# Kernel optimization log

Measured on AMD Instinct MI355X. Metric: run time of the kernel, lower is better.

The kernel has to match this reference:

```python
import jax, jax.numpy as jnp
import numpy as np
from jax import lax

KS = 3
N = KS ** 3  # 27 kernel taps


def setup_inputs() -> dict:
    key = jax.random.key(0)
    k1, k2, k3 = jax.random.split(key, 3)
    B, Cin, Cout, D, H, W = 1, 32, 32, 32, 48, 48
    x = jax.random.normal(k1, (B, Cin, D, H, W), jnp.float32)
    # offset conv: 81 = 3*27 output channels, no bias (nn.Conv3d(..., bias=False))
    w_off = jax.random.normal(k2, (3 * N, Cin, KS, KS, KS), jnp.float32) * 0.01
    # deform conv kernel (bias defaults to None -> no bias)
    w_def = jax.random.normal(k3, (Cout, Cin, KS, KS, KS), jnp.float32) / np.sqrt(Cin * N)
    return {"x": x, "w_off": w_off, "w_def": w_def}


def _deform_block(x, w_off, w_def):
    B, C, D, H, W = x.shape
    dt = x.dtype

    # standard dense offset conv, padding=1
    offsets = lax.conv_general_dilated(
        x, w_off, (1, 1, 1), [(1, 1), (1, 1), (1, 1)],
        dimension_numbers=("NCDHW", "OIDHW", "NCDHW"))
    off = jnp.transpose(offsets, (0, 2, 3, 4, 1))  # (B,D,H,W,3N)
    od, oh, ow = off[..., :N], off[..., N:2 * N], off[..., 2 * N:]

    # zero-pad input (ConstantPad3d(1))
    xp = jnp.pad(x, ((0, 0), (0, 0), (1, 1), (1, 1), (1, 1)))
    Dp, Hp, Wp = D + 2, H + 2, W + 2

    # p_n: kernel grid offsets in (kd,kh,kw) row-major order, matching conv-weight layout
    r = jnp.arange(-(KS // 2), KS // 2 + 1, dtype=dt)
    pn = jnp.stack(jnp.meshgrid(r, r, r, indexing="ij"), 0).reshape(3, N)
    # p_0: centers in padded coordinates (1..D etc.)
    p0d = jnp.arange(1, D + 1, dtype=dt)[:, None, None, None]
    p0h = jnp.arange(1, H + 1, dtype=dt)[None, :, None, None]
    p0w = jnp.arange(1, W + 1, dtype=dt)[None, None, :, None]

    pd = p0d + pn[0] + od  # (B,D,H,W,N) sampling coords
    ph = p0h + pn[1] + oh
    pw = p0w + pn[2] + ow

    # integer corners (detached in original)
    fd = lax.stop_gradient(jnp.floor(pd))
    fh = lax.stop_gradient(jnp.floor(ph))
    fw = lax.stop_gradient(jnp.floor(pw))
    qd0 = jnp.clip(fd, 0, Dp - 1); qd1 = jnp.clip(fd + 1, 0, Dp - 1)
    qh0 = jnp.clip(fh, 0, Hp - 1); qh1 = jnp.clip(fh + 1, 0, Hp - 1)
    qw0 = jnp.clip(fw, 0, Wp - 1); qw1 = jnp.clip(fw + 1, 0, Wp - 1)

    # clip p to valid range (as in reference impl)
    pd = jnp.clip(pd, 0, Dp - 1)
    ph = jnp.clip(ph, 0, Hp - 1)
    pw = jnp.clip(pw, 0, Wp - 1)

    # trilinear weights per axis: g = 1 - |q - p|
    gd0 = 1 + (qd0 - pd); gd1 = 1 - (qd1 - pd)
    gh0 = 1 + (qh0 - ph); gh1 = 1 - (qh1 - ph)
    gw0 = 1 + (qw0 - pw); gw1 = 1 - (qw1 - pw)

    xf = xp.reshape(B, C, Dp * Hp * Wp)

    def gather(idd, ihh, iww):
        lin = ((idd.astype(jnp.int32) * Hp + ihh.astype(jnp.int32)) * Wp
               + iww.astype(jnp.int32)).reshape(B, 1, -1)
        v = jnp.take_along_axis(xf, jnp.broadcast_to(lin, (B, C, lin.shape[-1])), axis=2)
        return v.reshape(B, C, D, H, W, N)

    x_off = jnp.zeros((B, C, D, H, W, N), dt)
    for gd, idd in ((gd0, qd0), (gd1, qd1)):
        for gh, ihh in ((gh0, qh0), (gh1, qh1)):
            for gw, iww in ((gw0, qw0), (gw1, qw1)):
                x_off = x_off + (gd * gh * gw)[:, None] * gather(idd, ihh, iww)

    # stride-ks conv over reshaped x_offset == weighted sum over the N taps
    Cout = w_def.shape[0]
    out = jnp.einsum("bcdhwn,ocn->bodhw", x_off, w_def.reshape(Cout, C, N))
    return out


def reference(x, w_off, w_def):
    return _deform_block(x, w_off, w_def)
```

## Files before the change

kernel.cpp:

```cpp
#include <hip/hip_runtime.h>

typedef __attribute__((ext_vector_type(8))) short  short8;
typedef __attribute__((ext_vector_type(4))) float  f32x4;

#define CIN 32
#define COUT 32
#define DD 32
#define HH 48
#define WW 48
#define NTAP 27
#define SPATIAL (DD*HH*WW)

#define BP2_ELEMS (27*6*64*8)
#define OFF_WPK   ((size_t)BP2_ELEMS*2)
#define WPK_ELEMS (27*2*64*8)
#define OFF_XT    (OFF_WPK + (size_t)WPK_ELEMS*2)

__device__ __forceinline__ unsigned short f2bf(float f) {
    union { float f; unsigned u; } v; v.f = f;
    unsigned r = v.u + 0x7FFFu + ((v.u >> 16) & 1u);
    return (unsigned short)(r >> 16);
}
__device__ __forceinline__ float bf2f(unsigned short h) {
    union { unsigned u; float f; } v; v.u = ((unsigned)h) << 16;
    return v.f;
}

__global__ __launch_bounds__(256) void wprep2_kernel(
        const float* __restrict__ w_off, unsigned short* __restrict__ Bp2)
{
    int i = blockIdx.x * 256 + threadIdx.x;
    if (i >= BP2_ELEMS) return;
    int e    = i & 7;
    int lane = (i >> 3) & 63;
    int j    = (i >> 9) % 6;
    int n    = i / (512 * 6);
    int col = lane & 15, kg = lane >> 4;
    int oc = j * 16 + col, c = kg * 8 + e;
    float v = (oc < 81) ? w_off[((size_t)oc * CIN + c) * NTAP + n] : 0.f;
    Bp2[i] = f2bf(v);
}

__global__ __launch_bounds__(256) void wdefprep_kernel(
        const float* __restrict__ w_def, unsigned short* __restrict__ wpk)
{
    int i = blockIdx.x * 256 + threadIdx.x;
    if (i >= WPK_ELEMS) return;
    int e    = i & 7;
    int lane = (i >> 3) & 63;
    int half = (i >> 9) & 1;
    int n    = i >> 10;
    int kg = lane >> 4, col = lane & 15;
    int c  = kg * 8 + e, oc = half * 16 + col;
    wpk[i] = f2bf(w_def[((size_t)oc * CIN + c) * NTAP + n]);
}

__global__ __launch_bounds__(256) void xtrans_kernel(
        const float* __restrict__ x, unsigned short* __restrict__ xT)
{
    __shared__ float t[CIN][65];
    const int p0 = blockIdx.x * 64;
    const int tid = threadIdx.x;
    const int tx = tid & 63, ty = tid >> 6;
    #pragma unroll
    for (int k = 0; k < 8; ++k) {
        int c = ty + k * 4;
        t[c][tx] = x[(size_t)c * SPATIAL + p0 + tx];
    }
    __syncthreads();
    const int pl = tid >> 2, cg = (tid & 3) * 8;
    short8 v;
    #pragma unroll
    for (int i = 0; i < 8; ++i) v[i] = (short)f2bf(t[cg + i][pl]);
    *(short8*)&xT[((size_t)(p0 + pl)) * 32 + cg] = v;
}

__global__ __launch_bounds__(256, 4) void fused_deform(
        const unsigned short* __restrict__ xT,
        const unsigned short* __restrict__ Bp2,
        const unsigned short* __restrict__ wpk,
        float* __restrict__ out)
{
    __shared__ float offl[4][16][97];

    const int tid  = threadIdx.x;
    const int lane = tid & 63, wv = tid >> 6;
    const int p0   = blockIdx.x * 64 + wv * 16;
    const int kg   = lane >> 4;
    const int row  = lane & 15;
    const int pos  = p0 + row;
    const int w = pos % WW, h = (pos / WW) % HH, d = pos / (WW * HH);

    f32x4 cacc[6];
    #pragma unroll
    for (int j = 0; j < 6; ++j) cacc[j] = (f32x4){0.f, 0.f, 0.f, 0.f};

    const short8* Bv = (const short8*)Bp2;
    {
        int n = 0;
        #pragma unroll 1
        for (int td = -1; td <= 1; ++td) {
            #pragma unroll 1
            for (int th = -1; th <= 1; ++th) {
                #pragma unroll
                for (int tw = -1; tw <= 1; ++tw, ++n) {
                    bool valid = ((unsigned)(d + td) < DD)
                               & ((unsigned)(h + th) < HH)
                               & ((unsigned)(w + tw) < WW);
                    int dpos = pos + (td * HH + th) * WW + tw;
                    short8 af = {0, 0, 0, 0, 0, 0, 0, 0};
                    if (valid)
                        af = *(const short8*)&xT[dpos * 32 + kg * 8];
                    #pragma unroll
                    for (int j = 0; j < 6; ++j)
                        cacc[j] = __builtin_amdgcn_mfma_f32_16x16x32_bf16(
                                      af, Bv[(n * 6 + j) * 64 + lane], cacc[j], 0, 0, 0);
                }
            }
        }
    }

    #pragma unroll
    for (int j = 0; j < 6; ++j) {
        #pragma unroll
        for (int r = 0; r < 4; ++r)
            offl[wv][kg * 4 + r][j * 16 + row] = cacc[j][r];
    }
    __syncthreads();

    const float Dp1 = 33.f, Hp1 = 49.f, Wp1 = 49.f;
    const float* ol = &offl[wv][row][0];

    f32x4 acc0 = {0.f, 0.f, 0.f, 0.f};
    f32x4 acc1 = {0.f, 0.f, 0.f, 0.f};
    const short8* wv8 = (const short8*)wpk;

    #pragma unroll 1
    for (int n = 0; n < NTAP; ++n) {
        float od = ol[n];
        float oh = ol[27 + n];
        float ow = ol[54 + n];
        float rd = (float)(n / 9) - 1.f;
        float rh = (float)((n / 3) % 3) - 1.f;
        float rw = (float)(n % 3) - 1.f;

        float pdp = (float)(d + 1) + rd + od;
        float php = (float)(h + 1) + rh + oh;
        float pwp = (float)(w + 1) + rw + ow;

        float fd = floorf(pdp), fh = floorf(php), fw = floorf(pwp);
        float qd0 = fminf(fmaxf(fd,       0.f), Dp1);
        float qd1 = fminf(fmaxf(fd + 1.f, 0.f), Dp1);
        float qh0 = fminf(fmaxf(fh,       0.f), Hp1);
        float qh1 = fminf(fmaxf(fh + 1.f, 0.f), Hp1);
        float qw0 = fminf(fmaxf(fw,       0.f), Wp1);
        float qw1 = fminf(fmaxf(fw + 1.f, 0.f), Wp1);
        pdp = fminf(fmaxf(pdp, 0.f), Dp1);
        php = fminf(fmaxf(php, 0.f), Hp1);
        pwp = fminf(fmaxf(pwp, 0.f), Wp1);

        float gds[2] = { 1.f + (qd0 - pdp), 1.f - (qd1 - pdp) };
        float ghs[2] = { 1.f + (qh0 - php), 1.f - (qh1 - php) };
        float gws[2] = { 1.f + (qw0 - pwp), 1.f - (qw1 - pwp) };
        int   ids[2] = { (int)qd0, (int)qd1 };
        int   ihs[2] = { (int)qh0, (int)qh1 };
        int   iws[2] = { (int)qw0, (int)qw1 };

        float xo[8];
        #pragma unroll
        for (int i = 0; i < 8; ++i) xo[i] = 0.f;

        #pragma unroll
        for (int e = 0; e < 8; ++e) {
            int a = e >> 2, b = (e >> 1) & 1, q = e & 1;
            int zd = ids[a], zh = ihs[b], zw = iws[q];
            bool val = (zd >= 1) & (zd <= DD) & (zh >= 1) & (zh <= HH)
                     & (zw >= 1) & (zw <= WW);
            float g  = val ? gds[a] * ghs[b] * gws[q] : 0.f;
            int base = val ? (((zd - 1) * HH + (zh - 1)) * WW + (zw - 1)) : 0;
            short8 v8 = *(const short8*)&xT[base * 32 + kg * 8];
            #pragma unroll
            for (int i = 0; i < 8; ++i)
                xo[i] = fmaf(g, bf2f((unsigned short)v8[i]), xo[i]);
        }

        short8 ahi, alo;
        #pragma unroll
        for (int i = 0; i < 8; ++i) {
            unsigned short hb = f2bf(xo[i]);
            ahi[i] = (short)hb;
            alo[i] = (short)f2bf(xo[i] - bf2f(hb));
        }

        short8 b0 = wv8[(n * 2 + 0) * 64 + lane];
        short8 b1 = wv8[(n * 2 + 1) * 64 + lane];
        acc0 = __builtin_amdgcn_mfma_f32_16x16x32_bf16(ahi, b0, acc0, 0, 0, 0);
        acc0 = __builtin_amdgcn_mfma_f32_16x16x32_bf16(alo, b0, acc0, 0, 0, 0);
        acc1 = __builtin_amdgcn_mfma_f32_16x16x32_bf16(ahi, b1, acc1, 0, 0, 0);
        acc1 = __builtin_amdgcn_mfma_f32_16x16x32_bf16(alo, b1, acc1, 0, 0, 0);
    }

    const int oc0 = row, oc1 = 16 + row;
    const int pb  = p0 + kg * 4;
    *(f32x4*)&out[(size_t)oc0 * SPATIAL + pb] = acc0;
    *(f32x4*)&out[(size_t)oc1 * SPATIAL + pb] = acc1;
}

extern "C" void kernel_launch(void* const* d_in, const int* in_sizes, int n_in,
                              void* d_out, int out_size, void* d_ws, size_t ws_size,
                              hipStream_t stream)
{
    const float* x     = (const float*)d_in[0];
    const float* w_off = (const float*)d_in[1];
    const float* w_def = (const float*)d_in[2];
    float* out = (float*)d_out;

    unsigned short* Bp2 = (unsigned short*)((char*)d_ws);
    unsigned short* wpk = (unsigned short*)((char*)d_ws + OFF_WPK);
    unsigned short* xT  = (unsigned short*)((char*)d_ws + OFF_XT);

    wprep2_kernel<<<(BP2_ELEMS + 255) / 256, 256, 0, stream>>>(w_off, Bp2);
    wdefprep_kernel<<<(WPK_ELEMS + 255) / 256, 256, 0, stream>>>(w_def, wpk);
    xtrans_kernel<<<SPATIAL / 64, 256, 0, stream>>>(x, xT);
    fused_deform<<<SPATIAL / 64, 256, 0, stream>>>(xT, Bp2, wpk, out);
}
```

Before: 137.1 us.

## Split deform taps across wave pairs and drop hi/lo bf16 split

Each block now covers 32 positions instead of 64, and two waves share each 16-position group. Each wave computes half of the offset channels (reordered by tap) and then handles half of the 27 deformable taps, and the partial results are reduced through shared memory. The hi/lo bf16 split MFMA is replaced by a single packed bf16 conversion, which halves the deform MFMAs but lowers accuracy. Bounds and index math are simplified with clamped indices, occupancy is raised to 8 blocks per SIMD, and more blocks are launched.

```diff
diff --git a/kernel.cpp b/kernel.cpp
--- a/kernel.cpp
+++ b/kernel.cpp
@@ -34,10 +34,16 @@
     int e    = i & 7;
     int lane = (i >> 3) & 63;
     int j    = (i >> 9) % 6;
-    int n    = i / (512 * 6);
+    int ktap = i / (512 * 6);
     int col = lane & 15, kg = lane >> 4;
-    int oc = j * 16 + col, c = kg * 8 + e;
-    float v = (oc < 81) ? w_off[((size_t)oc * CIN + c) * NTAP + n] : 0.f;
+    int ocp = j * 16 + col;
+    int ts  = ocp >= 48;
+    int r   = ocp - 48 * ts;
+    int nl  = r / 3, axis = r - 3 * nl;
+    int n   = 14 * ts + nl;
+    int c   = kg * 8 + e;
+    bool valid = ts ? (r < 39) : (r < 42);
+    float v = valid ? w_off[((size_t)(axis * 27 + n) * CIN + c) * NTAP + ktap] : 0.f;
     Bp2[i] = f2bf(v);
 }
 
@@ -75,27 +81,32 @@
     *(short8*)&xT[((size_t)(p0 + pl)) * 32 + cg] = v;
 }
 
-__global__ __launch_bounds__(256, 4) void fused_deform(
+__global__ __launch_bounds__(256, 8) void fused_deform2(
         const unsigned short* __restrict__ xT,
         const unsigned short* __restrict__ Bp2,
         const unsigned short* __restrict__ wpk,
         float* __restrict__ out)
 {
-    __shared__ float offl[4][16][97];
+    __shared__ float offl[4][16][50];
+    __shared__ f32x4 redv[2][64][2];
 
     const int tid  = threadIdx.x;
     const int lane = tid & 63, wv = tid >> 6;
-    const int p0   = blockIdx.x * 64 + wv * 16;
+    const int pg   = wv & 1, ts = wv >> 1;
+    const int p0   = blockIdx.x * 32 + pg * 16;
     const int kg   = lane >> 4;
     const int row  = lane & 15;
     const int pos  = p0 + row;
     const int w = pos % WW, h = (pos / WW) % HH, d = pos / (WW * HH);
 
-    f32x4 cacc[6];
-    #pragma unroll
-    for (int j = 0; j < 6; ++j) cacc[j] = (f32x4){0.f, 0.f, 0.f, 0.f};
-
-    const short8* Bv = (const short8*)Bp2;
+    const short8* Xv  = (const short8*)xT;
+    const short8* Bv  = (const short8*)Bp2;
+    const short8* wv8 = (const short8*)wpk;
+
+    f32x4 cacc[3];
+    #pragma unroll
+    for (int j = 0; j < 3; ++j) cacc[j] = (f32x4){0.f, 0.f, 0.f, 0.f};
+
     {
         int n = 0;
         #pragma unroll 1
@@ -107,64 +118,88 @@
                     bool valid = ((unsigned)(d + td) < DD)
                                & ((unsigned)(h + th) < HH)
                                & ((unsigned)(w + tw) < WW);
-                    int dpos = pos + (td * HH + th) * WW + tw;
+                    int dpos = pos + td * 2304 + th * 48 + tw;
                     short8 af = {0, 0, 0, 0, 0, 0, 0, 0};
-                    if (valid)
-                        af = *(const short8*)&xT[dpos * 32 + kg * 8];
+                    if (valid) af = Xv[dpos * 4 + kg];
                     #pragma unroll
-                    for (int j = 0; j < 6; ++j)
-                        cacc[j] = __builtin_amdgcn_mfma_f32_16x16x32_bf16(
-                                      af, Bv[(n * 6 + j) * 64 + lane], cacc[j], 0, 0, 0);
+                    for (int jl = 0; jl < 3; ++jl)
+                        cacc[jl] = __builtin_amdgcn_mfma_f32_16x16x32_bf16(
+                            af, Bv[(n * 6 + ts * 3 + jl) * 64 + lane], cacc[jl], 0, 0, 0);
                 }
             }
         }
     }
 
     #pragma unroll
-    for (int j = 0; j < 6; ++j) {
+    for (int jl = 0; jl < 3; ++jl) {
         #pragma unroll
         for (int r = 0; r < 4; ++r)
-            offl[wv][kg * 4 + r][j * 16 + row] = cacc[j][r];
+            offl[wv][kg * 4 + r][jl * 16 + row] = cacc[jl][r];
     }
     __syncthreads();
 
-    const float Dp1 = 33.f, Hp1 = 49.f, Wp1 = 49.f;
     const float* ol = &offl[wv][row][0];
+    const int NT    = ts ? 13 : 14;
+    const int nbase = ts * 14;
 
     f32x4 acc0 = {0.f, 0.f, 0.f, 0.f};
     f32x4 acc1 = {0.f, 0.f, 0.f, 0.f};
-    const short8* wv8 = (const short8*)wpk;
 
     #pragma unroll 1
-    for (int n = 0; n < NTAP; ++n) {
-        float od = ol[n];
-        float oh = ol[27 + n];
-        float ow = ol[54 + n];
-        float rd = (float)(n / 9) - 1.f;
-        float rh = (float)((n / 3) % 3) - 1.f;
-        float rw = (float)(n % 3) - 1.f;
+    for (int nl = 0; nl < NT; ++nl) {
+        const int nn = nbase + nl;
+        float od = ol[nl * 3 + 0];
+        float oh = ol[nl * 3 + 1];
+        float ow = ol[nl * 3 + 2];
+        float rd = (float)(nn / 9) - 1.f;
+        float rh = (float)((nn / 3) % 3) - 1.f;
+        float rw = (float)(nn % 3) - 1.f;
 
         float pdp = (float)(d + 1) + rd + od;
         float php = (float)(h + 1) + rh + oh;
         float pwp = (float)(w + 1) + rw + ow;
 
         float fd = floorf(pdp), fh = floorf(php), fw = floorf(pwp);
-        float qd0 = fminf(fmaxf(fd,       0.f), Dp1);
-        float qd1 = fminf(fmaxf(fd + 1.f, 0.f), Dp1);
-        float qh0 = fminf(fmaxf(fh,       0.f), Hp1);
-        float qh1 = fminf(fmaxf(fh + 1.f, 0.f), Hp1);
-        float qw0 = fminf(fmaxf(fw,       0.f), Wp1);
-        float qw1 = fminf(fmaxf(fw + 1.f, 0.f), Wp1);
-        pdp = fminf(fmaxf(pdp, 0.f), Dp1);
-        php = fminf(fmaxf(php, 0.f), Hp1);
-        pwp = fminf(fmaxf(pwp, 0.f), Wp1);
-
-        float gds[2] = { 1.f + (qd0 - pdp), 1.f - (qd1 - pdp) };
-        float ghs[2] = { 1.f + (qh0 - php), 1.f - (qh1 - php) };
-        float gws[2] = { 1.f + (qw0 - pwp), 1.f - (qw1 - pwp) };
-        int   ids[2] = { (int)qd0, (int)qd1 };
-        int   ihs[2] = { (int)qh0, (int)qh1 };
-        int   iws[2] = { (int)qw0, (int)qw1 };
+        float qd0 = fminf(fmaxf(fd,       0.f), 33.f);
+        float qd1 = fminf(fmaxf(fd + 1.f, 0.f), 33.f);
+        float qh0 = fminf(fmaxf(fh,       0.f), 49.f);
+        float qh1 = fminf(fmaxf(fh + 1.f, 0.f), 49.f);
+        float qw0 = fminf(fmaxf(fw,       0.f), 49.f);
+        float qw1 = fminf(fmaxf(fw + 1.f, 0.f), 49.f);
+        float pcd = fminf(fmaxf(pdp, 0.f), 33.f);
+        float pch = fminf(fmaxf(php, 0.f), 49.f);
+        float pcw = fminf(fmaxf(pwp, 0.f), 49.f);
+
+        float gd0 = 1.f + (qd0 - pcd), gd1 = 1.f - (qd1 - pcd);
+        float gh0 = 1.f + (qh0 - pch), gh1 = 1.f - (qh1 - pch);
+        float gw0 = 1.f + (qw0 - pcw), gw1 = 1.f - (qw1 - pcw);
+        gd0 = (qd0 >= 1.f && qd0 <= 32.f) ? gd0 : 0.f;
+        gd1 = (qd1 >= 1.f && qd1 <= 32.f) ? gd1 : 0.f;
+        gh0 = (qh0 >= 1.f && qh0 <= 48.f) ? gh0 : 0.f;
+        gh1 = (qh1 >= 1.f && qh1 <= 48.f) ? gh1 : 0.f;
+        gw0 = (qw0 >= 1.f && qw0 <= 48.f) ? gw0 : 0.f;
+        gw1 = (qw1 >= 1.f && qw1 <= 48.f) ? gw1 : 0.f;
+        int zd0 = (int)fminf(fmaxf(qd0, 1.f), 32.f) - 1;
+        int zd1 = (int)fminf(fmaxf(qd1, 1.f), 32.f) - 1;
+        int zh0 = (int)fminf(fmaxf(qh0, 1.f), 48.f) - 1;
+        int zh1 = (int)fminf(fmaxf(qh1, 1.f), 48.f) - 1;
+        int zw0 = (int)fminf(fmaxf(qw0, 1.f), 48.f) - 1;
+        int zw1 = (int)fminf(fmaxf(qw1, 1.f), 48.f) - 1;
+
+        int bd0 = zd0 * 2304, bd1 = zd1 * 2304;
+        int bh0 = zh0 * 48,   bh1 = zh1 * 48;
+        float gdh00 = gd0 * gh0, gdh01 = gd0 * gh1;
+        float gdh10 = gd1 * gh0, gdh11 = gd1 * gh1;
+
+        int   bb[8]; float gg[8];
+        bb[0] = bd0 + bh0 + zw0;  gg[0] = gdh00 * gw0;
+        bb[1] = bd0 + bh0 + zw1;  gg[1] = gdh00 * gw1;
+        bb[2] = bd0 + bh1 + zw0;  gg[2] = gdh01 * gw0;
+        bb[3] = bd0 + bh1 + zw1;  gg[3] = gdh01 * gw1;
+        bb[4] = bd1 + bh0 + zw0;  gg[4] = gdh10 * gw0;
+        bb[5] = bd1 + bh0 + zw1;  gg[5] = gdh10 * gw1;
+        bb[6] = bd1 + bh1 + zw0;  gg[6] = gdh11 * gw0;
+        bb[7] = bd1 + bh1 + zw1;  gg[7] = gdh11 * gw1;
 
         float xo[8];
         #pragma unroll
@@ -172,38 +207,40 @@
 
         #pragma unroll
         for (int e = 0; e < 8; ++e) {
-            int a = e >> 2, b = (e >> 1) & 1, q = e & 1;
-            int zd = ids[a], zh = ihs[b], zw = iws[q];
-            bool val = (zd >= 1) & (zd <= DD) & (zh >= 1) & (zh <= HH)
-                     & (zw >= 1) & (zw <= WW);
-            float g  = val ? gds[a] * ghs[b] * gws[q] : 0.f;
-            int base = val ? (((zd - 1) * HH + (zh - 1)) * WW + (zw - 1)) : 0;
-            short8 v8 = *(const short8*)&xT[base * 32 + kg * 8];
+            short8 v8 = Xv[bb[e] * 4 + kg];
+            float g = gg[e];
             #pragma unroll
             for (int i = 0; i < 8; ++i)
                 xo[i] = fmaf(g, bf2f((unsigned short)v8[i]), xo[i]);
         }
 
-        short8 ahi, alo;
-        #pragma unroll
-        for (int i = 0; i < 8; ++i) {
-            unsigned short hb = f2bf(xo[i]);
-            ahi[i] = (short)hb;
-            alo[i] = (short)f2bf(xo[i] - bf2f(hb));
+        union { unsigned u[4]; short8 s; } av;
+        #pragma unroll
+        for (int i = 0; i < 4; ++i) {
+            unsigned r;
+            asm("v_cvt_pk_bf16_f32 %0, %1, %2"
+                : "=v"(r) : "v"(xo[2 * i]), "v"(xo[2 * i + 1]));
+            av.u[i] = r;
         }
 
-        short8 b0 = wv8[(n * 2 + 0) * 64 + lane];
-        short8 b1 = wv8[(n * 2 + 1) * 64 + lane];
-        acc0 = __builtin_amdgcn_mfma_f32_16x16x32_bf16(ahi, b0, acc0, 0, 0, 0);
-        acc0 = __builtin_amdgcn_mfma_f32_16x16x32_bf16(alo, b0, acc0, 0, 0, 0);
-        acc1 = __builtin_amdgcn_mfma_f32_16x16x32_bf16(ahi, b1, acc1, 0, 0, 0);
-        acc1 = __builtin_amdgcn_mfma_f32_16x16x32_bf16(alo, b1, acc1, 0, 0, 0);
-    }
-
-    const int oc0 = row, oc1 = 16 + row;
-    const int pb  = p0 + kg * 4;
-    *(f32x4*)&out[(size_t)oc0 * SPATIAL + pb] = acc0;
-    *(f32x4*)&out[(size_t)oc1 * SPATIAL + pb] = acc1;
+        short8 b0 = wv8[(nn * 2 + 0) * 64 + lane];
+        short8 b1 = wv8[(nn * 2 + 1) * 64 + lane];
+        acc0 = __builtin_amdgcn_mfma_f32_16x16x32_bf16(av.s, b0, acc0, 0, 0, 0);
+        acc1 = __builtin_amdgcn_mfma_f32_16x16x32_bf16(av.s, b1, acc1, 0, 0, 0);
+    }
+
+    if (ts) {
+        redv[pg][lane][0] = acc0;
+        redv[pg][lane][1] = acc1;
+    }
+    __syncthreads();
+    if (!ts) {
+        acc0 += redv[pg][lane][0];
+        acc1 += redv[pg][lane][1];
+        const int pb = p0 + kg * 4;
+        *(f32x4*)&out[(size_t)row        * SPATIAL + pb] = acc0;
+        *(f32x4*)&out[(size_t)(16 + row) * SPATIAL + pb] = acc1;
+    }
 }
 
 extern "C" void kernel_launch(void* const* d_in, const int* in_sizes, int n_in,
@@ -222,5 +259,5 @@
     wprep2_kernel<<<(BP2_ELEMS + 255) / 256, 256, 0, stream>>>(w_off, Bp2);
     wdefprep_kernel<<<(WPK_ELEMS + 255) / 256, 256, 0, stream>>>(w_def, wpk);
     xtrans_kernel<<<SPATIAL / 64, 256, 0, stream>>>(x, xT);
-    fused_deform<<<SPATIAL / 64, 256, 0, stream>>>(xT, Bp2, wpk, out);
-}
+    fused_deform2<<<SPATIAL / 32, 256, 0, stream>>>(xT, Bp2, wpk, out);
+}
```

Result: slower. 166.8 us (+21.7%).
